# Performance work log

Measured on AMD Instinct MI355X. Metric: run time of the kernel, lower is better.

Reference implementation:

```python
import jax, jax.numpy as jnp
import numpy as np

K = 8  # search_range in sample_wise_recolor
BIG = 1e30


def setup_inputs() -> dict:
    key = jax.random.key(0)
    ks = jax.random.split(key, 6)
    L, N = 16384, 10000  # L: upsampled candidate voxels (multiple of 8), N: target points
    pred_F = jax.random.normal(ks[0], (L,), jnp.float32)
    cand_xyz = jax.random.normal(ks[1], (L, 3), jnp.float32) * 50.0
    cand_rgb = jax.random.uniform(ks[2], (L, 3), jnp.float32)
    tgt_xyz = jax.random.normal(ks[3], (N, 3), jnp.float32) * 50.0
    tgt_rgb = jax.random.uniform(ks[4], (N, 3), jnp.float32)
    keep_target = jax.random.randint(ks[5], (L,), 0, 2, jnp.int32)
    return {"pred_F": pred_F, "cand_xyz": cand_xyz, "cand_rgb": cand_rgb,
            "tgt_xyz": tgt_xyz, "tgt_rgb": tgt_rgb, "keep_target": keep_target,
            "points_num": 8192}


def _get_keep(pred, points_num):
    # local-max mask over groups of 8 children (scatter of per-row argmax)
    L = pred.shape[0]
    p8 = pred.reshape(-1, 8)
    rows = jnp.arange(p8.shape[0])
    is_local_max = jnp.zeros(p8.shape, dtype=bool).at[rows, jnp.argmax(p8, axis=1)].set(True).reshape(-1)
    # kthvalue over the non-local-max subset: local-max entries pushed to +inf so the
    # k-th smallest of the full sorted array equals the k-th smallest of the subset.
    k = L - points_num  # static python int
    vals = jnp.where(is_local_max, jnp.inf, pred)
    threshold = jnp.sort(vals)[k - 1]
    return (pred > threshold) | is_local_max


def _pairwise_sqdist(a, b):
    # a: [P,3], b: [Q,3] -> [P,Q] squared distances
    a2 = jnp.sum(a * a, axis=1)
    b2 = jnp.sum(b * b, axis=1)
    d2 = a2[:, None] + b2[None, :] - 2.0 * (a @ b.T)
    return jnp.maximum(d2, 0.0)


def _recolor_loss(cand_xyz, rgb, keep, tgt_xyz, tgt_rgb):
    L = cand_xyz.shape[0]
    N = tgt_xyz.shape[0]
    d2 = _pairwise_sqdist(tgt_xyz, cand_xyz)  # [N, L]

    # ---- recolor_backward: KNN from each target point into kept candidates ----
    d_masked = jnp.where(keep[None, :], d2, BIG)
    neg_d, idx = jax.lax.top_k(-d_masked, K)  # [N, K]
    d = -neg_d
    zero_mask = d == 0.0
    min_mask = (d == jnp.min(d, axis=1, keepdims=True)) & ~jnp.any(zero_mask, axis=1)[:, None]
    w = jnp.where(min_mask, 1.0 / jnp.sqrt(jnp.maximum(d, 1e-30)), 0.0)  # [N, K]

    flat_idx = idx.reshape(-1)
    num = jnp.zeros((L, 3), rgb.dtype).at[flat_idx].add((tgt_rgb[:, None, :] * w[:, :, None]).reshape(-1, 3))
    den = jnp.zeros((L,), rgb.dtype).at[flat_idx].add(w.reshape(-1))
    has_den = den != 0.0
    recolored = jnp.where(has_den[:, None], num / jnp.where(has_den, den, 1.0)[:, None], 0.0)

    # exact-match (zero-distance) targets overwrite; scatter with safe out-of-range dummy row
    safe_idx = jnp.where(zero_mask, idx, L).reshape(-1)
    tgt_exp = jnp.broadcast_to(tgt_rgb[:, None, :], (N, K, 3)).reshape(-1, 3)
    recolored = jnp.concatenate([recolored, jnp.zeros((1, 3), rgb.dtype)], 0).at[safe_idx].set(tgt_exp)[:L]
    empty = jnp.concatenate([~has_den, jnp.zeros((1,), bool)], 0).at[safe_idx].set(False)[:L]
    empty = empty & keep  # only kept candidates matter

    # ---- recolor_forward: kept candidates with no color yet pull from nearest targets ----
    neg_df, idxf = jax.lax.top_k(-d2.T, K)  # [L, K]
    df = -neg_df
    mf = df == jnp.min(df, axis=1, keepdims=True)
    rec_fwd = jnp.sum(tgt_rgb[idxf] * mf[:, :, None], axis=1) / jnp.sum(mf, axis=1, keepdims=True).astype(rgb.dtype)
    recolored = jnp.where(empty[:, None], rec_fwd, recolored)

    # L1 loss over kept candidates only; recolor target is no-grad in the original
    recolored = jax.lax.stop_gradient(recolored)
    return jnp.sum(jnp.where(keep[:, None], jnp.abs(rgb - recolored), 0.0))


def reference(pred_F, cand_xyz, cand_rgb, tgt_xyz, tgt_rgb, keep_target, points_num):
    keep = _get_keep(jax.lax.stop_gradient(pred_F), points_num)  # @torch.no_grad
    # coord recon loss: BCE-with-logits, reduction='sum'
    t = keep_target.astype(pred_F.dtype)
    coord_loss = jnp.sum(jnp.maximum(pred_F, 0.0) - pred_F * t + jnp.log1p(jnp.exp(-jnp.abs(pred_F))))
    # inverse_transform_for_color in training mode: x * 255
    rgb = cand_rgb * 255.0
    rgb_loss = _recolor_loss(cand_xyz, rgb, keep, tgt_xyz, tgt_rgb)
    return jnp.stack([coord_loss, rgb_loss])
```

## Files before the change

kernel.cpp:

```cpp
#include <hip/hip_runtime.h>
#include <hip/hip_bf16.h>


#define SCAN_T 256
#define CHUNK  128
typedef unsigned long long ull;

__device__ __forceinline__ void select_bin(
    unsigned int* hist, int nb, unsigned int rank,
    unsigned int* sB, unsigned int* sR, int tid) {
  if (tid < 64) {
    int g = nb >> 6;
    unsigned int sum = 0;
    for (int j = 0; j < g; ++j) sum += hist[tid * g + j];
    unsigned int incl = sum;
    for (int o = 1; o < 64; o <<= 1) {
      unsigned int v = __shfl_up(incl, o);
      if (tid >= o) incl += v;
    }
    unsigned int excl = incl - sum;
    bool cond = (rank >= excl) && (rank < incl);
    unsigned long long bal = __ballot(cond);
    int first = __ffsll((long long)bal) - 1;
    if (tid == first) {
      unsigned int r = rank - excl, cum = 0;
      for (int j = 0; j < g; ++j) {
        unsigned int c = hist[tid * g + j];
        if (r < cum + c) { *sB = (unsigned int)(tid * g + j); *sR = r - cum; break; }
        cum += c;
      }
    }
  }
}

__global__ __launch_bounds__(512) void k_init_sel(
    const float* __restrict__ pred, const float* __restrict__ txyz,
    const int* __restrict__ pnum_p,
    float4* __restrict__ ttile, float4* __restrict__ numden,
    int* __restrict__ zerohit, ull* __restrict__ tmin, ull* __restrict__ fmin,
    unsigned char* __restrict__ islm, int* __restrict__ counters,
    float* __restrict__ out, float* __restrict__ thr_out,
    int L, int N, int IB) {
  __shared__ unsigned int skey[16384];
  __shared__ unsigned int hist[2048];
  __shared__ unsigned int sB, sR;
  int tid = threadIdx.x;

  if ((int)blockIdx.x < IB) {
    int gidx = blockIdx.x * 512 + tid;
    int gsz = IB * 512;
    for (int i = gidx; i < N; i += gsz) {
      float x = txyz[3*i], y = txyz[3*i+1], z = txyz[3*i+2];
      ttile[i] = make_float4(x, y, z, fmaf(x, x, fmaf(y, y, z * z)));
      tmin[i] = ~0ull;
    }
    for (int i = gidx; i < L; i += gsz) {
      numden[i] = make_float4(0.f, 0.f, 0.f, 0.f);
      zerohit[i] = 0;
      fmin[i] = ~0ull;
    }
    if (gidx < 8) counters[gidx] = 0;
    if (gidx < 2) out[gidx] = 0.f;
    return;
  }

  int ngroups = L >> 3;
  for (int g = tid; g < ngroups; g += 512) {
    const float4* pv = (const float4*)pred + (size_t)g * 2;
    float4 a = pv[0], b = pv[1];
    float v[8] = {a.x, a.y, a.z, a.w, b.x, b.y, b.z, b.w};
    int bi = 0; float bv = v[0];
    #pragma unroll
    for (int j = 1; j < 8; ++j) if (v[j] > bv) { bv = v[j]; bi = j; }
    ull lmpack = 0ull;
    #pragma unroll
    for (int j = 0; j < 8; ++j) {
      unsigned int fb = __float_as_uint(v[j]);
      unsigned int mk = (fb & 0x80000000u) ? ~fb : (fb | 0x80000000u);
      if (j == bi) { mk = 0xFF800000u; lmpack |= 1ull << (8 * j); }
      skey[g * 8 + j] = mk;
    }
    *(ull*)(islm + (size_t)g * 8) = lmpack;
  }
  __syncthreads();

  unsigned int rank = (unsigned int)(L - pnum_p[0] - 1);
  const uint4* s4 = (const uint4*)skey;
  int n4 = L >> 2;
  for (int b = tid; b < 2048; b += 512) hist[b] = 0u;
  __syncthreads();
  for (int i = tid; i < n4; i += 512) {
    uint4 v = s4[i];
    atomicAdd(&hist[v.x >> 21], 1u); atomicAdd(&hist[v.y >> 21], 1u);
    atomicAdd(&hist[v.z >> 21], 1u); atomicAdd(&hist[v.w >> 21], 1u);
  }
  __syncthreads();
  select_bin(hist, 2048, rank, &sB, &sR, tid);
  __syncthreads();
  unsigned int B1 = sB, R1 = sR;
  for (int b = tid; b < 2048; b += 512) hist[b] = 0u;
  __syncthreads();
  for (int i = tid; i < n4; i += 512) {
    uint4 v = s4[i];
    if ((v.x >> 21) == B1) atomicAdd(&hist[(v.x >> 10) & 2047u], 1u);
    if ((v.y >> 21) == B1) atomicAdd(&hist[(v.y >> 10) & 2047u], 1u);
    if ((v.z >> 21) == B1) atomicAdd(&hist[(v.z >> 10) & 2047u], 1u);
    if ((v.w >> 21) == B1) atomicAdd(&hist[(v.w >> 10) & 2047u], 1u);
  }
  __syncthreads();
  select_bin(hist, 2048, R1, &sB, &sR, tid);
  __syncthreads();
  unsigned int B2 = sB, R2 = sR;
  for (int b = tid; b < 1024; b += 512) hist[b] = 0u;
  __syncthreads();
  unsigned int top22 = (B1 << 11) | B2;
  for (int i = tid; i < n4; i += 512) {
    uint4 v = s4[i];
    if ((v.x >> 10) == top22) atomicAdd(&hist[v.x & 1023u], 1u);
    if ((v.y >> 10) == top22) atomicAdd(&hist[v.y & 1023u], 1u);
    if ((v.z >> 10) == top22) atomicAdd(&hist[v.z & 1023u], 1u);
    if ((v.w >> 10) == top22) atomicAdd(&hist[v.w & 1023u], 1u);
  }
  __syncthreads();
  select_bin(hist, 1024, R2, &sB, &sR, tid);
  __syncthreads();
  if (tid == 0) {
    unsigned int fkey = (B1 << 21) | (B2 << 10) | sB;
    unsigned int fb = (fkey & 0x80000000u) ? (fkey & 0x7FFFFFFFu) : ~fkey;
    thr_out[0] = __uint_as_float(fb);
  }
}

__global__ __launch_bounds__(256) void k_keepc(
    const float* __restrict__ pred, const unsigned char* __restrict__ islm,
    const float* __restrict__ thr_p, const float* __restrict__ cxyz,
    const int* __restrict__ ktgt, int* __restrict__ keep,
    float4* __restrict__ klist, int* __restrict__ kidx,
    int* __restrict__ counters, float* __restrict__ out, int L) {
  int i = blockIdx.x * 256 + threadIdx.x;
  float thr = thr_p[0];
  float term = 0.f;
  if (i < L) {
    float p = pred[i];
    bool kp = (p > thr) || islm[i];
    keep[i] = kp ? 1 : 0;
    if (kp) {
      int pos = atomicAdd(&counters[0], 1);
      float x = cxyz[3*i], y = cxyz[3*i+1], z = cxyz[3*i+2];
      klist[pos] = make_float4(x, y, z, fmaf(x, x, fmaf(y, y, z * z)));
      kidx[pos] = i;
    }
    float t = (float)ktgt[i];
    term = fmaxf(p, 0.f) - p * t + log1pf(expf(-fabsf(p)));
  }
  for (int o = 32; o > 0; o >>= 1) term += __shfl_down(term, o);
  if ((threadIdx.x & 63) == 0) atomicAdd(&out[0], term);
}

__global__ __launch_bounds__(SCAN_T) void k_scan2(
    const float* __restrict__ txyz, const float4* __restrict__ klist,
    const int* __restrict__ kidx, const float4* __restrict__ ttile,
    const int* __restrict__ counters, ull* __restrict__ tmin,
    ull* __restrict__ fmin, int L, int N, int YB) {
  __shared__ float4 tile[CHUNK];
  int tid = threadIdx.x, x = blockIdx.x, y = blockIdx.y;
  int kc = counters[0];

  if (y < YB) {
    int c0 = y * CHUNK;
    if (x * 1024 >= N || c0 >= kc) return;
    int cnt = min(CHUNK, kc - c0);
    if (tid < cnt) tile[tid] = klist[c0 + tid];
    __syncthreads();
    int tb = x * 1024 + tid;
    float ntx[4], nty[4], ntz[4], best[4];
    int bpos[4];
    bool act[4];
    #pragma unroll
    for (int j = 0; j < 4; ++j) {
      int t = tb + 256 * j;
      act[j] = t < N;
      float tx = 0.f, ty = 0.f, tz = 0.f;
      if (act[j]) { tx = txyz[3*t]; ty = txyz[3*t+1]; tz = txyz[3*t+2]; }
      ntx[j] = -2.f * tx; nty[j] = -2.f * ty; ntz[j] = -2.f * tz;
      best[j] = 3e38f; bpos[j] = 0;
    }
    #pragma unroll 4
    for (int c = 0; c < cnt; ++c) {
      float4 cd = tile[c];
      #pragma unroll
      for (int j = 0; j < 4; ++j) {
        float d = fmaf(ntx[j], cd.x, cd.w);
        d = fmaf(nty[j], cd.y, d);
        d = fmaf(ntz[j], cd.z, d);
        if (d < best[j]) { best[j] = d; bpos[j] = c; }
      }
    }
    #pragma unroll
    for (int j = 0; j < 4; ++j) {
      if (act[j]) {
        int p = c0 + bpos[j];
        float4 cd = klist[p];
        float tx = -0.5f * ntx[j], ty = -0.5f * nty[j], tz = -0.5f * ntz[j];
        float dx = tx - cd.x, dy = ty - cd.y, dz = tz - cd.z;
        float dtrue = fmaf(dx, dx, fmaf(dy, dy, dz * dz));
        ull pack = ((ull)__float_as_uint(dtrue) << 32) | (unsigned int)kidx[p];
        atomicMin(&tmin[tb + 256 * j], pack);
      }
    }
  } else {
    int t0 = (y - YB) * CHUNK;
    if (x * 1024 >= kc || t0 >= N) return;
    int tcnt = min(CHUNK, N - t0);
    if (tid < tcnt) tile[tid] = ttile[t0 + tid];
    __syncthreads();
    int eb = x * 1024 + tid;
    float ncx[4], ncy[4], ncz[4], c2[4], best[4];
    int bpos[4], li[4];
    bool act[4];
    #pragma unroll
    for (int j = 0; j < 4; ++j) {
      int e = eb + 256 * j;
      act[j] = e < kc;
      float cx = 0.f, cy = 0.f, cz = 0.f;
      c2[j] = 0.f; li[j] = 0;
      if (act[j]) {
        float4 cd = klist[e];
        cx = cd.x; cy = cd.y; cz = cd.z; c2[j] = cd.w;
        li[j] = kidx[e];
      }
      ncx[j] = -2.f * cx; ncy[j] = -2.f * cy; ncz[j] = -2.f * cz;
      best[j] = 3e38f; bpos[j] = 0;
    }
    #pragma unroll 4
    for (int c = 0; c < tcnt; ++c) {
      float4 td = tile[c];
      #pragma unroll
      for (int j = 0; j < 4; ++j) {
        float d = fmaf(ncx[j], td.x, td.w);
        d = fmaf(ncy[j], td.y, d);
        d = fmaf(ncz[j], td.z, d);
        if (d < best[j]) { best[j] = d; bpos[j] = c; }
      }
    }
    #pragma unroll
    for (int j = 0; j < 4; ++j) {
      if (act[j]) {
        float dkey = fmaxf(best[j] + c2[j], 0.f);
        ull pack = ((ull)__float_as_uint(dkey) << 32) |
                   (unsigned int)(t0 + bpos[j]);
        atomicMin(&fmin[li[j]], pack);
      }
    }
  }
}

__global__ __launch_bounds__(256) void k_scatter(
    const float* __restrict__ trgb, const ull* __restrict__ tmin,
    float4* __restrict__ numden, int* __restrict__ zerohit,
    float4* __restrict__ zcolor, int N) {
  int t = blockIdx.x * 256 + threadIdx.x;
  if (t >= N) return;
  ull pack = tmin[t];
  float d = __uint_as_float((unsigned int)(pack >> 32));
  int idx = (int)(pack & 0xFFFFFFFFull);
  float r = trgb[3*t], g = trgb[3*t+1], b = trgb[3*t+2];
  if (d == 0.0f) {
    zerohit[idx] = 1;
    zcolor[idx] = make_float4(r, g, b, 0.f);
  } else {
    float w = 1.0f / sqrtf(fmaxf(d, 1e-30f));
    atomicAdd(&numden[idx].x, r * w);
    atomicAdd(&numden[idx].y, g * w);
    atomicAdd(&numden[idx].z, b * w);
    atomicAdd(&numden[idx].w, w);
  }
}

__global__ __launch_bounds__(256) void k_loss(
    const float* __restrict__ crgb, const float* __restrict__ trgb,
    const int* __restrict__ keep, const float4* __restrict__ numden,
    const int* __restrict__ zerohit, const float4* __restrict__ zcolor,
    const ull* __restrict__ fmin, float* __restrict__ out, int L) {
  int l = blockIdx.x * 256 + threadIdx.x;
  float loss = 0.f;
  if (l < L && keep[l]) {
    float rr, rg, rb;
    if (zerohit[l]) {
      float4 z = zcolor[l]; rr = z.x; rg = z.y; rb = z.z;
    } else {
      float4 nd = numden[l];
      if (nd.w != 0.f) { rr = nd.x / nd.w; rg = nd.y / nd.w; rb = nd.z / nd.w; }
      else {
        int ti = (int)(fmin[l] & 0xFFFFFFFFull);
        rr = trgb[3*ti]; rg = trgb[3*ti+1]; rb = trgb[3*ti+2];
      }
    }
    float sr = crgb[3*l]*255.f, sg = crgb[3*l+1]*255.f, sb = crgb[3*l+2]*255.f;
    loss = fabsf(sr - rr) + fabsf(sg - rg) + fabsf(sb - rb);
  }
  for (int o = 32; o > 0; o >>= 1) loss += __shfl_down(loss, o);
  if ((threadIdx.x & 63) == 0) atomicAdd(&out[1], loss);
}

extern "C" void kernel_launch(void* const* d_in, const int* in_sizes, int n_in,
                              void* d_out, int out_size, void* d_ws, size_t ws_size,
                              hipStream_t stream) {
  const float* pred = (const float*)d_in[0];
  const float* cxyz = (const float*)d_in[1];
  const float* crgb = (const float*)d_in[2];
  const float* txyz = (const float*)d_in[3];
  const float* trgb = (const float*)d_in[4];
  const int*   ktgt = (const int*)d_in[5];
  const int*   pnum = (const int*)d_in[6];
  int L = in_sizes[0];
  int N = in_sizes[3] / 3;

  char* ws = (char*)d_ws;
  size_t off = 0;
  float4* klist  = (float4*)(ws + off);   off += (size_t)L * 16;
  float4* ttile  = (float4*)(ws + off);   off += (size_t)((N + 3) & ~3) * 16;
  float4* numden = (float4*)(ws + off);   off += (size_t)L * 16;
  float4* zcolor = (float4*)(ws + off);   off += (size_t)L * 16;
  ull* tmin      = (ull*)(ws + off);      off += (size_t)((N + 1) & ~1) * 8;
  ull* fmin      = (ull*)(ws + off);      off += (size_t)L * 8;
  int* keep      = (int*)(ws + off);      off += (size_t)L * 4;
  int* kidx      = (int*)(ws + off);      off += (size_t)L * 4;
  int* zerohit   = (int*)(ws + off);      off += (size_t)L * 4;
  float* thr_slot = (float*)(ws + off);   off += 16;
  int* counters  = (int*)(ws + off);      off += 256;
  unsigned char* islm = (unsigned char*)(ws + off); off += ((size_t)L + 15) & ~15ull;
  float* out = (float*)d_out;

  int nbL = (L + 255) / 256;
  int nbN = (N + 255) / 256;
  int mx = max(L, N);

  int IB = (mx + 511) / 512;
  k_init_sel<<<IB + 1, 512, 0, stream>>>(
      pred, txyz, pnum, ttile, numden, zerohit, tmin, fmin, islm, counters,
      out, thr_slot, L, N, IB);

  k_keepc<<<nbL, 256, 0, stream>>>(
      pred, islm, thr_slot, cxyz, ktgt, keep, klist, kidx, counters, out, L);

  int gx = (mx + 1023) / 1024;
  int YB = (L + CHUNK - 1) / CHUNK;
  int YF = (N + CHUNK - 1) / CHUNK;
  dim3 gs(gx, YB + YF);
  k_scan2<<<gs, SCAN_T, 0, stream>>>(
      txyz, klist, kidx, ttile, counters, tmin, fmin, L, N, YB);

  k_scatter<<<nbN, 256, 0, stream>>>(trgb, tmin, numden, zerohit, zcolor, N);

  k_loss<<<nbL, 256, 0, stream>>>(
      crgb, trgb, keep, numden, zerohit, zcolor, fmin, out, L);
}
```

Before: 132.4 us.

## Fuse keep-compaction into selection kernel with an intra-grid flag wait

The separate k_keepc launch is removed. The init blocks of k_init_sel now spin on a global release/acquire flag set by the selection block, then compute keep, the compacted kept list and the BCE loss themselves. Block size goes from 512 to 1024 threads, and a memset resets the flag before each launch. This saves one kernel launch but depends on the selection block being co-resident with the spinning blocks, and the spin-wait can deadlock or serialize if it is not.

```diff
diff --git a/kernel.cpp b/kernel.cpp
--- a/kernel.cpp
+++ b/kernel.cpp
@@ -33,22 +33,25 @@
   }
 }
 
-__global__ __launch_bounds__(512) void k_init_sel(
+__global__ __launch_bounds__(1024) void k_init_sel(
     const float* __restrict__ pred, const float* __restrict__ txyz,
+    const float* __restrict__ cxyz, const int* __restrict__ ktgt,
     const int* __restrict__ pnum_p,
     float4* __restrict__ ttile, float4* __restrict__ numden,
     int* __restrict__ zerohit, ull* __restrict__ tmin, ull* __restrict__ fmin,
-    unsigned char* __restrict__ islm, int* __restrict__ counters,
-    float* __restrict__ out, float* __restrict__ thr_out,
+    unsigned char* __restrict__ islm, int* __restrict__ keep,
+    float4* __restrict__ klist, int* __restrict__ kidx,
+    int* counters, float* __restrict__ out, float* __restrict__ thr_out,
     int L, int N, int IB) {
   __shared__ unsigned int skey[16384];
   __shared__ unsigned int hist[2048];
   __shared__ unsigned int sB, sR;
+  __shared__ float s_thr;
   int tid = threadIdx.x;
 
   if ((int)blockIdx.x < IB) {
-    int gidx = blockIdx.x * 512 + tid;
-    int gsz = IB * 512;
+    int gidx = blockIdx.x * 1024 + tid;
+    int gsz = IB * 1024;
     for (int i = gidx; i < N; i += gsz) {
       float x = txyz[3*i], y = txyz[3*i+1], z = txyz[3*i+2];
       ttile[i] = make_float4(x, y, z, fmaf(x, x, fmaf(y, y, z * z)));
@@ -59,13 +62,35 @@
       zerohit[i] = 0;
       fmin[i] = ~0ull;
     }
-    if (gidx < 8) counters[gidx] = 0;
-    if (gidx < 2) out[gidx] = 0.f;
+    if (tid == 0) {
+      while (__hip_atomic_load(&counters[15], __ATOMIC_ACQUIRE,
+                               __HIP_MEMORY_SCOPE_AGENT) == 0)
+        __builtin_amdgcn_s_sleep(8);
+      s_thr = thr_out[0];
+    }
+    __syncthreads();
+    float thr = s_thr;
+    float term = 0.f;
+    for (int i = gidx; i < L; i += gsz) {
+      float p = pred[i];
+      bool kp = (p > thr) || islm[i];
+      keep[i] = kp ? 1 : 0;
+      if (kp) {
+        int pos = atomicAdd(&counters[0], 1);
+        float x = cxyz[3*i], y = cxyz[3*i+1], z = cxyz[3*i+2];
+        klist[pos] = make_float4(x, y, z, fmaf(x, x, fmaf(y, y, z * z)));
+        kidx[pos] = i;
+      }
+      float t = (float)ktgt[i];
+      term += fmaxf(p, 0.f) - p * t + log1pf(expf(-fabsf(p)));
+    }
+    for (int o = 32; o > 0; o >>= 1) term += __shfl_down(term, o);
+    if ((tid & 63) == 0) atomicAdd(&out[0], term);
     return;
   }
 
   int ngroups = L >> 3;
-  for (int g = tid; g < ngroups; g += 512) {
+  for (int g = tid; g < ngroups; g += 1024) {
     const float4* pv = (const float4*)pred + (size_t)g * 2;
     float4 a = pv[0], b = pv[1];
     float v[8] = {a.x, a.y, a.z, a.w, b.x, b.y, b.z, b.w};
@@ -87,9 +112,9 @@
   unsigned int rank = (unsigned int)(L - pnum_p[0] - 1);
   const uint4* s4 = (const uint4*)skey;
   int n4 = L >> 2;
-  for (int b = tid; b < 2048; b += 512) hist[b] = 0u;
-  __syncthreads();
-  for (int i = tid; i < n4; i += 512) {
+  for (int b = tid; b < 2048; b += 1024) hist[b] = 0u;
+  __syncthreads();
+  for (int i = tid; i < n4; i += 1024) {
     uint4 v = s4[i];
     atomicAdd(&hist[v.x >> 21], 1u); atomicAdd(&hist[v.y >> 21], 1u);
     atomicAdd(&hist[v.z >> 21], 1u); atomicAdd(&hist[v.w >> 21], 1u);
@@ -98,9 +123,9 @@
   select_bin(hist, 2048, rank, &sB, &sR, tid);
   __syncthreads();
   unsigned int B1 = sB, R1 = sR;
-  for (int b = tid; b < 2048; b += 512) hist[b] = 0u;
-  __syncthreads();
-  for (int i = tid; i < n4; i += 512) {
+  for (int b = tid; b < 2048; b += 1024) hist[b] = 0u;
+  __syncthreads();
+  for (int i = tid; i < n4; i += 1024) {
     uint4 v = s4[i];
     if ((v.x >> 21) == B1) atomicAdd(&hist[(v.x >> 10) & 2047u], 1u);
     if ((v.y >> 21) == B1) atomicAdd(&hist[(v.y >> 10) & 2047u], 1u);
@@ -111,10 +136,10 @@
   select_bin(hist, 2048, R1, &sB, &sR, tid);
   __syncthreads();
   unsigned int B2 = sB, R2 = sR;
-  for (int b = tid; b < 1024; b += 512) hist[b] = 0u;
+  for (int b = tid; b < 1024; b += 1024) hist[b] = 0u;
   __syncthreads();
   unsigned int top22 = (B1 << 11) | B2;
-  for (int i = tid; i < n4; i += 512) {
+  for (int i = tid; i < n4; i += 1024) {
     uint4 v = s4[i];
     if ((v.x >> 10) == top22) atomicAdd(&hist[v.x & 1023u], 1u);
     if ((v.y >> 10) == top22) atomicAdd(&hist[v.y & 1023u], 1u);
@@ -128,33 +153,14 @@
     unsigned int fkey = (B1 << 21) | (B2 << 10) | sB;
     unsigned int fb = (fkey & 0x80000000u) ? (fkey & 0x7FFFFFFFu) : ~fkey;
     thr_out[0] = __uint_as_float(fb);
-  }
-}
-
-__global__ __launch_bounds__(256) void k_keepc(
-    const float* __restrict__ pred, const unsigned char* __restrict__ islm,
-    const float* __restrict__ thr_p, const float* __restrict__ cxyz,
-    const int* __restrict__ ktgt, int* __restrict__ keep,
-    float4* __restrict__ klist, int* __restrict__ kidx,
-    int* __restrict__ counters, float* __restrict__ out, int L) {
-  int i = blockIdx.x * 256 + threadIdx.x;
-  float thr = thr_p[0];
-  float term = 0.f;
-  if (i < L) {
-    float p = pred[i];
-    bool kp = (p > thr) || islm[i];
-    keep[i] = kp ? 1 : 0;
-    if (kp) {
-      int pos = atomicAdd(&counters[0], 1);
-      float x = cxyz[3*i], y = cxyz[3*i+1], z = cxyz[3*i+2];
-      klist[pos] = make_float4(x, y, z, fmaf(x, x, fmaf(y, y, z * z)));
-      kidx[pos] = i;
-    }
-    float t = (float)ktgt[i];
-    term = fmaxf(p, 0.f) - p * t + log1pf(expf(-fabsf(p)));
-  }
-  for (int o = 32; o > 0; o >>= 1) term += __shfl_down(term, o);
-  if ((threadIdx.x & 63) == 0) atomicAdd(&out[0], term);
+    out[0] = 0.f; out[1] = 0.f;
+    #pragma unroll
+    for (int c = 0; c < 8; ++c) counters[c] = 0;
+  }
+  __syncthreads();
+  if (tid == 0)
+    __hip_atomic_store(&counters[15], 1, __ATOMIC_RELEASE,
+                       __HIP_MEMORY_SCOPE_AGENT);
 }
 
 __global__ __launch_bounds__(SCAN_T) void k_scan2(
@@ -336,13 +342,12 @@
   int nbN = (N + 255) / 256;
   int mx = max(L, N);
 
-  int IB = (mx + 511) / 512;
-  k_init_sel<<<IB + 1, 512, 0, stream>>>(
-      pred, txyz, pnum, ttile, numden, zerohit, tmin, fmin, islm, counters,
-      out, thr_slot, L, N, IB);
-
-  k_keepc<<<nbL, 256, 0, stream>>>(
-      pred, islm, thr_slot, cxyz, ktgt, keep, klist, kidx, counters, out, L);
+  hipMemsetAsync((void*)(counters + 15), 0, 4, stream);
+
+  int IB = (mx + 1023) / 1024;
+  k_init_sel<<<IB + 1, 1024, 0, stream>>>(
+      pred, txyz, cxyz, ktgt, pnum, ttile, numden, zerohit, tmin, fmin,
+      islm, keep, klist, kidx, counters, out, thr_slot, L, N, IB);
 
   int gx = (mx + 1023) / 1024;
   int YB = (L + CHUNK - 1) / CHUNK;
```

Result: no change. 132.6 us (median of 3 runs) (+0.2%).
